# Optimization experiments

Measured on AMD Instinct MI355X. Metric: run time of the kernel, lower is better.

## Reference

```python
import jax, jax.numpy as jnp
import numpy as np

N_NODES = 50000
N_EDGES = 800000
N_GRAPHS = 64
EMB_DIM = 24
N_KERNELS = 2
M_DIM = 64
FOURIER = 4
POS_DIM = 3
EDGE_IN = 2 * FOURIER + 1 + 2 * EMB_DIM  # 57
MLP_DIM = 256
N_OUT = 4
FFNN_IN = EMB_DIM * (N_KERNELS + 1)  # 72


def _lin(key, fan_in, fan_out, stack=None):
    # xavier-uniform weight, zero bias (matches weights_init)
    lim = (6.0 / (fan_in + fan_out)) ** 0.5
    shp = ((stack,) if stack else ()) + (fan_in, fan_out)
    w = jax.random.uniform(key, shp, minval=-lim, maxval=lim, dtype=jnp.float32)
    b = jnp.zeros(((stack,) if stack else ()) + (fan_out,), jnp.float32)
    return w, b


def setup_inputs() -> dict:
    key = jax.random.key(0)
    ks = jax.random.split(key, 20)
    z = jax.random.randint(ks[0], (N_NODES,), 0, 22)
    pos = jax.random.normal(ks[1], (N_NODES, POS_DIM), jnp.float32)
    edge_index = jax.random.randint(ks[2], (2, N_EDGES), 0, N_NODES)
    batch_idx = jnp.sort(jax.random.randint(ks[3], (N_NODES,), 0, N_GRAPHS))
    lim_e = (6.0 / (22 + EMB_DIM)) ** 0.5
    emb_table = jax.random.uniform(ks[4], (22, EMB_DIM), minval=-lim_e, maxval=lim_e, dtype=jnp.float32)
    emb_w, emb_b = _lin(ks[5], EMB_DIM, EMB_DIM)
    # EGNN kernel params, stacked over N_KERNELS
    ew1, eb1 = _lin(ks[6], EDGE_IN, EDGE_IN * 2, N_KERNELS)
    ew2, eb2 = _lin(ks[7], EDGE_IN * 2, M_DIM, N_KERNELS)
    cw1, cb1 = _lin(ks[8], M_DIM, M_DIM * 4, N_KERNELS)
    cw2, cb2 = _lin(ks[9], M_DIM * 4, 1, N_KERNELS)
    nw1, nb1 = _lin(ks[10], EMB_DIM + M_DIM, EMB_DIM * 2, N_KERNELS)
    nw2, nb2 = _lin(ks[11], EMB_DIM * 2, EMB_DIM, N_KERNELS)
    # ffnn: Linear(72,256), Linear(256,256), Linear(256,256), Linear(256,4)
    f0w, f0b = _lin(ks[12], FFNN_IN, MLP_DIM)
    f1w, f1b = _lin(ks[13], MLP_DIM, MLP_DIM)
    f2w, f2b = _lin(ks[14], MLP_DIM, MLP_DIM)
    fow, fob = _lin(ks[15], MLP_DIM, N_OUT)
    return dict(z=z, pos=pos, edge_index=edge_index, batch_idx=batch_idx,
                emb_table=emb_table, emb_w=emb_w, emb_b=emb_b,
                ew1=ew1, eb1=eb1, ew2=ew2, eb2=eb2,
                cw1=cw1, cb1=cb1, cw2=cw2, cb2=cb2,
                nw1=nw1, nb1=nb1, nw2=nw2, nb2=nb2,
                f0w=f0w, f0b=f0b, f1w=f1w, f1b=f1b, f2w=f2w, f2b=f2b,
                fow=fow, fob=fob)


def _egnn_layer(feats, coors, src, dst, ew1, eb1, ew2, eb2, cw1, cb1, cw2, cb2, nw1, nb1, nw2, nb2):
    # EGNN_sparse (PyG flow source_to_target: i=dst=edge_index[1], j=src=edge_index[0])
    rel = coors[src] - coors[dst]                       # [E,3]
    d = jnp.sum(rel * rel, axis=-1, keepdims=True)      # [E,1] squared distance
    scales = 2.0 ** jnp.arange(FOURIER, dtype=feats.dtype)
    ds = d / scales                                     # [E,4]
    edge_feat = jnp.concatenate([jnp.sin(ds), jnp.cos(ds), d], axis=-1)  # [E,9]
    e_in = jnp.concatenate([feats[dst], feats[src], edge_feat], axis=-1)  # [E,57]
    m_ij = jax.nn.silu(jax.nn.silu(e_in @ ew1 + eb1) @ ew2 + eb2)         # [E,64]
    coor_w = jax.nn.silu(m_ij @ cw1 + cb1) @ cw2 + cb2                    # [E,1]
    coors_out = coors + jax.ops.segment_sum(coor_w * rel, dst, num_segments=N_NODES)
    m_i = jax.ops.segment_sum(m_ij, dst, num_segments=N_NODES)            # [N,64]
    h = jax.nn.silu(jnp.concatenate([feats, m_i], axis=-1) @ nw1 + nb1)
    feats_out = feats + (h @ nw2 + nb2)
    return feats_out, coors_out


def reference(z, pos, edge_index, batch_idx, emb_table, emb_w, emb_b,
              ew1, eb1, ew2, eb2, cw1, cb1, cw2, cb2, nw1, nb1, nw2, nb2,
              f0w, f0b, f1w, f1b, f2w, f2b, fow, fob):
    src, dst = edge_index[0], edge_index[1]
    feats = emb_table[z] @ emb_w + emb_b
    coors = pos
    flist = [feats]
    for k in range(N_KERNELS):
        feats, coors = _egnn_layer(feats, coors, src, dst,
                                   ew1[k], eb1[k], ew2[k], eb2[k],
                                   cw1[k], cb1[k], cw2[k], cb2[k],
                                   nw1[k], nb1[k], nw2[k], nb2[k])
        flist.append(feats)
    x = jax.nn.silu(jnp.concatenate(flist, axis=-1))     # [N,72]
    x = jax.nn.silu(x @ f0w + f0b)
    x = jax.nn.silu(x @ f1w + f1b)
    x = jax.nn.silu(x @ f2w + f2b)                       # [N,256]
    cnt = jax.ops.segment_sum(jnp.ones((x.shape[0],), x.dtype), batch_idx, num_segments=N_GRAPHS)
    pooled = jax.ops.segment_sum(x, batch_idx, num_segments=N_GRAPHS) / jnp.maximum(cnt, 1.0)[:, None]
    return jax.nn.sigmoid(pooled @ fow + fob)            # [B,4]
```

## Files before the change

### kernel.cpp

```cpp
#include <hip/hip_runtime.h>
#include <hip/hip_bf16.h>

#define N_NODES  50000
#define N_EDGES  800000
#define N_GRAPHS 64
#define EMB      24
#define MDIM     64
#define EDGE_IN  57
#define EH       114
#define CH       256
#define NIN      88
#define NH       48
#define MLP      256
#define ETILE    128
#define NTILE    64

typedef __bf16 bf16_t;
typedef __bf16 bf16x8 __attribute__((ext_vector_type(8)));
typedef __bf16 bf16x4 __attribute__((ext_vector_type(4)));
typedef float  f32x4  __attribute__((ext_vector_type(4)));

__device__ __forceinline__ float siluf(float x) {
    return x * __builtin_amdgcn_rcpf(1.0f + __expf(-x));
}

__global__ void embed_kernel(const int* __restrict__ z, const float* __restrict__ table,
                             const float* __restrict__ w, const float* __restrict__ b,
                             const int* __restrict__ batch, float* __restrict__ f0,
                             bf16_t* __restrict__ fb0, float* __restrict__ cnt)
{
    int n = blockIdx.x * blockDim.x + threadIdx.x;
    if (n >= N_NODES) return;
    float r[EMB];
    const float4* tr = reinterpret_cast<const float4*>(table + z[n] * EMB);
    #pragma unroll
    for (int q = 0; q < 6; q++) {
        float4 v = tr[q];
        r[q*4] = v.x; r[q*4+1] = v.y; r[q*4+2] = v.z; r[q*4+3] = v.w;
    }
    float o[EMB];
    #pragma unroll
    for (int j = 0; j < EMB; j++) o[j] = b[j];
    #pragma unroll
    for (int i = 0; i < EMB; i++) {
        #pragma unroll
        for (int j = 0; j < EMB; j++) o[j] = fmaf(r[i], w[i*EMB + j], o[j]);
    }
    float4* dst = reinterpret_cast<float4*>(f0 + (size_t)n * EMB);
    #pragma unroll
    for (int q = 0; q < 6; q++) dst[q] = make_float4(o[q*4], o[q*4+1], o[q*4+2], o[q*4+3]);
    bf16x8* bdst = reinterpret_cast<bf16x8*>(fb0 + (size_t)n * EMB);
    #pragma unroll
    for (int q = 0; q < 3; q++) {
        bf16x8 pk;
        #pragma unroll
        for (int j = 0; j < 8; j++) pk[j] = (bf16_t)o[q*8 + j];
        bdst[q] = pk;
    }
    atomicAdd(&cnt[batch[n]], 1.0f);
}

#define PK_W1   (128*64)
#define PK_W2   (64*128)
#define PK_CW   (256*64)
#define PK_F0   (256*128)
#define PK_FM   (256*256)
#define PK_TOT  (2*PK_W1 + 2*PK_W2 + PK_CW + PK_F0 + 2*PK_FM)
__global__ void pack_kernel(const float* __restrict__ ew1, const float* __restrict__ eb1,
                            const float* __restrict__ ew2, const float* __restrict__ eb2,
                            const float* __restrict__ cw1, const float* __restrict__ f0w,
                            const float* __restrict__ f1w, const float* __restrict__ f2w,
                            bf16_t* __restrict__ pw)
{
    int idx = blockIdx.x * blockDim.x + threadIdx.x;
    if (idx >= PK_TOT) return;
    float v = 0.0f;
    if (idx < 2 * PK_W1) {
        int l = idx / PK_W1, r = idx - l * PK_W1;
        int n = r >> 6, k = r & 63;
        if (n < EH && k < EDGE_IN)       v = ew1[(l * EDGE_IN + k) * EH + n];
        else if (n < EH && k == EDGE_IN) v = eb1[l * EH + n];
    } else if (idx < 2 * PK_W1 + 2 * PK_W2) {
        int r0 = idx - 2 * PK_W1;
        int l = r0 / PK_W2, r = r0 - l * PK_W2;
        int n = r >> 7, k = r & 127;
        if (k < EH)       v = ew2[(l * EH + k) * MDIM + n];
        else if (k == EH) v = eb2[l * MDIM + n];
    } else if (idx < 2 * PK_W1 + 2 * PK_W2 + PK_CW) {
        int r = idx - (2 * PK_W1 + 2 * PK_W2);
        int n = r >> 6, k = r & 63;
        v = cw1[k * CH + n];
    } else if (idx < 2 * PK_W1 + 2 * PK_W2 + PK_CW + PK_F0) {
        int r = idx - (2 * PK_W1 + 2 * PK_W2 + PK_CW);
        int n = r >> 7, k = r & 127;
        if (k < 72) v = f0w[k * MLP + n];
    } else {
        int r0 = idx - (2 * PK_W1 + 2 * PK_W2 + PK_CW + PK_F0);
        int l = r0 / PK_FM, r = r0 - l * PK_FM;
        int n = r >> 8, k = r & 255;
        v = (l == 0) ? f1w[k * MLP + n] : f2w[k * MLP + n];
    }
    pw[idx] = (bf16_t)v;
}

__global__ void hist_kernel(const int* __restrict__ dst, int* __restrict__ deg)
{
    int e = blockIdx.x * blockDim.x + threadIdx.x;
    if (e < N_EDGES) atomicAdd(&deg[dst[e]], 1);
}

__global__ __launch_bounds__(1024)
void scan_kernel(const int* __restrict__ deg, int* __restrict__ cursor)
{
    __shared__ int part[1024];
    int t = threadIdx.x;
    const int PER = 49;
    int base = t * PER;
    int s = 0;
    for (int i = 0; i < PER; i++) {
        int p = base + i;
        if (p < N_NODES) s += deg[p];
    }
    part[t] = s;
    __syncthreads();
    for (int off = 1; off < 1024; off <<= 1) {
        int add = (t >= off) ? part[t - off] : 0;
        __syncthreads();
        part[t] += add;
        __syncthreads();
    }
    int run = (t > 0) ? part[t - 1] : 0;
    for (int i = 0; i < PER; i++) {
        int p = base + i;
        if (p < N_NODES) { cursor[p] = run; run += deg[p]; }
    }
}

__global__ void scatter_kernel(const int* __restrict__ src, const int* __restrict__ dst,
                               int* __restrict__ cursor, int* __restrict__ srcs_s,
                               int* __restrict__ dsts_s)
{
    int e = blockIdx.x * blockDim.x + threadIdx.x;
    if (e >= N_EDGES) return;
    int d = dst[e];
    int pos = atomicAdd(&cursor[d], 1);
    srcs_s[pos] = src[e];
    dsts_s[pos] = d;
}

template<int COOR>
__global__ __launch_bounds__(256, 4)
void edge_mfma(const bf16_t* __restrict__ fb, const float* __restrict__ coors,
               const int* __restrict__ srcs_s, const int* __restrict__ dsts_s,
               const bf16_t* __restrict__ W1t, const bf16_t* __restrict__ W2t,
               const bf16_t* __restrict__ CW1t, const float* __restrict__ cb1,
               const float* __restrict__ cw2, const float* __restrict__ cb2,
               float* __restrict__ m_i, float* __restrict__ cdelta)
{
    __shared__ __align__(16) char R1raw[ETILE * 64 * 4];
    __shared__ float s_rel[COOR ? ETILE * 3 : 4];
    __shared__ int   s_dst[ETILE];
    bf16_t* R1 = (bf16_t*)R1raw;
    float*  Mf32 = (float*)R1raw;

    const int t = threadIdx.x;
    const int w = t >> 6;
    const int l = t & 63;
    const int row0 = w * 32;
    const int ebase = blockIdx.x * ETILE;
    const int l15 = l & 15, l4 = l >> 4;

    {
        int e_loc = t >> 1, half = t & 1;
        int e = ebase + e_loc;
        int s = srcs_s[e], d = dsts_s[e];
        if (half == 0) {
            s_dst[e_loc] = d;
            const bf16x8* fp = reinterpret_cast<const bf16x8*>(fb + (size_t)d * EMB);
            #pragma unroll
            for (int g = 0; g < 3; g++)
                *(bf16x8*)&R1[e_loc*64 + (g ^ (e_loc & 7))*8] = fp[g];
        } else {
            const bf16x8* fp = reinterpret_cast<const bf16x8*>(fb + (size_t)s * EMB);
            #pragma unroll
            for (int g = 0; g < 3; g++)
                *(bf16x8*)&R1[e_loc*64 + ((g + 3) ^ (e_loc & 7))*8] = fp[g];
            float rx = coors[s*3+0] - coors[d*3+0];
            float ry = coors[s*3+1] - coors[d*3+1];
            float rz = coors[s*3+2] - coors[d*3+2];
            float d2 = rx*rx + ry*ry + rz*rz;
            if (COOR) { s_rel[e_loc*3+0] = rx; s_rel[e_loc*3+1] = ry; s_rel[e_loc*3+2] = rz; }
            bf16x8 p6, p7;
            p6[0]=(bf16_t)__sinf(d2);        p6[1]=(bf16_t)__sinf(d2*0.5f);
            p6[2]=(bf16_t)__sinf(d2*0.25f);  p6[3]=(bf16_t)__sinf(d2*0.125f);
            p6[4]=(bf16_t)__cosf(d2);        p6[5]=(bf16_t)__cosf(d2*0.5f);
            p6[6]=(bf16_t)__cosf(d2*0.25f);  p6[7]=(bf16_t)__cosf(d2*0.125f);
            p7[0]=(bf16_t)d2; p7[1]=(bf16_t)1.0f;
            p7[2]=(bf16_t)0.f; p7[3]=(bf16_t)0.f; p7[4]=(bf16_t)0.f;
            p7[5]=(bf16_t)0.f; p7[6]=(bf16_t)0.f; p7[7]=(bf16_t)0.f;
            *(bf16x8*)&R1[e_loc*64 + (6 ^ (e_loc & 7))*8] = p6;
            *(bf16x8*)&R1[e_loc*64 + (7 ^ (e_loc & 7))*8] = p7;
        }
    }
    __syncthreads();

    f32x4 acc1[2][8];
    #pragma unroll
    for (int et = 0; et < 2; et++)
        #pragma unroll
        for (int ft = 0; ft < 8; ft++) acc1[et][ft] = (f32x4){0.f,0.f,0.f,0.f};
    #pragma unroll
    for (int ks = 0; ks < 2; ks++) {
        bf16x8 bfrag[2];
        #pragma unroll
        for (int et = 0; et < 2; et++) {
            int e = row0 + et*16 + l15;
            bfrag[et] = *(const bf16x8*)&R1[e*64 + ((ks*4 + l4) ^ (e & 7))*8];
        }
        #pragma unroll
        for (int ft = 0; ft < 8; ft++) {
            bf16x8 a = *(const bf16x8*)&W1t[(ft*16 + l15)*64 + (ks*4 + l4)*8];
            acc1[0][ft] = __builtin_amdgcn_mfma_f32_16x16x32_bf16(a, bfrag[0], acc1[0][ft], 0, 0, 0);
            acc1[1][ft] = __builtin_amdgcn_mfma_f32_16x16x32_bf16(a, bfrag[1], acc1[1][ft], 0, 0, 0);
        }
    }
    __syncthreads();
    #pragma unroll
    for (int et = 0; et < 2; et++)
        #pragma unroll
        for (int ft = 0; ft < 8; ft++) {
            int e = row0 + et*16 + l15;
            int f0 = ft*16 + l4*4;
            bf16x4 pk;
            #pragma unroll
            for (int r4 = 0; r4 < 4; r4++) {
                float hv = siluf(acc1[et][ft][r4]);
                if (f0 + r4 == EH) hv = 1.0f;
                pk[r4] = (bf16_t)hv;
            }
            *(bf16x4*)&R1[e*128 + ((f0 >> 3) ^ (e & 7))*8 + (f0 & 7)] = pk;
        }
    __syncthreads();

    f32x4 acc2[2][4];
    #pragma unroll
    for (int et = 0; et < 2; et++)
        #pragma unroll
        for (int ft = 0; ft < 4; ft++) acc2[et][ft] = (f32x4){0.f,0.f,0.f,0.f};
    #pragma unroll
    for (int ks = 0; ks < 4; ks++) {
        bf16x8 bfrag[2];
        #pragma unroll
        for (int et = 0; et < 2; et++) {
            int e = row0 + et*16 + l15;
            bfrag[et] = *(const bf16x8*)&R1[e*128 + ((ks*4 + l4) ^ (e & 7))*8];
        }
        #pragma unroll
        for (int ft = 0; ft < 4; ft++) {
            bf16x8 a = *(const bf16x8*)&W2t[(ft*16 + l15)*128 + (ks*4 + l4)*8];
            acc2[0][ft] = __builtin_amdgcn_mfma_f32_16x16x32_bf16(a, bfrag[0], acc2[0][ft], 0, 0, 0);
            acc2[1][ft] = __builtin_amdgcn_mfma_f32_16x16x32_bf16(a, bfrag[1], acc2[1][ft], 0, 0, 0);
        }
    }
    __syncthreads();
    #pragma unroll
    for (int et = 0; et < 2; et++)
        #pragma unroll
        for (int ft = 0; ft < 4; ft++) {
            int e = row0 + et*16 + l15;
            int f0 = ft*16 + l4*4;
            f32x4 v;
            #pragma unroll
            for (int r4 = 0; r4 < 4; r4++) v[r4] = siluf(acc2[et][ft][r4]);
            *(f32x4*)&Mf32[e*64 + (((f0 >> 2) ^ (e & 7)) << 2)] = v;
        }
    __syncthreads();

    {
        int col = t & 63;
        int gsw_base = col >> 2, cw = col & 3;
        int gb = w * 32;
        int cur = s_dst[gb];
        float run = 0.f;
        for (int i = 0; i < 32; i++) {
            int row = gb + i;
            int d = s_dst[row];
            float v = Mf32[row*64 + ((gsw_base ^ (row & 7)) << 2) + cw];
            if (d != cur) { atomicAdd(&m_i[(size_t)cur*64 + col], run); run = 0.f; cur = d; }
            run += v;
        }
        atomicAdd(&m_i[(size_t)cur*64 + col], run);
    }

    if (COOR) {
        float csum[2] = {0.f, 0.f};
        #pragma unroll
        for (int half = 0; half < 2; half++) {
            f32x4 acc3[2][8];
            #pragma unroll
            for (int et = 0; et < 2; et++)
                #pragma unroll
                for (int ft = 0; ft < 8; ft++) acc3[et][ft] = (f32x4){0.f,0.f,0.f,0.f};
            #pragma unroll
            for (int ks = 0; ks < 2; ks++) {
                bf16x8 bfrag[2];
                #pragma unroll
                for (int et = 0; et < 2; et++) {
                    int e = row0 + et*16 + l15;
                    int g0 = (ks*4 + l4) * 2;
                    f32x4 lo = *(const f32x4*)&Mf32[e*64 + ((g0 ^ (e & 7)) << 2)];
                    f32x4 hi = *(const f32x4*)&Mf32[e*64 + (((g0 + 1) ^ (e & 7)) << 2)];
                    bf16x8 bk;
                    #pragma unroll
                    for (int j = 0; j < 4; j++) { bk[j] = (bf16_t)lo[j]; bk[j+4] = (bf16_t)hi[j]; }
                    bfrag[et] = bk;
                }
                #pragma unroll
                for (int ft = 0; ft < 8; ft++) {
                    bf16x8 a = *(const bf16x8*)&CW1t[(half*128 + ft*16 + l15)*64 + (ks*4 + l4)*8];
                    acc3[0][ft] = __builtin_amdgcn_mfma_f32_16x16x32_bf16(a, bfrag[0], acc3[0][ft], 0, 0, 0);
                    acc3[1][ft] = __builtin_amdgcn_mfma_f32_16x16x32_bf16(a, bfrag[1], acc3[1][ft], 0, 0, 0);
                }
            }
            #pragma unroll
            for (int ft = 0; ft < 8; ft++) {
                int f0 = half*128 + ft*16 + l4*4;
                float4 c1 = *(const float4*)&cb1[f0];
                float4 w2 = *(const float4*)&cw2[f0];
                #pragma unroll
                for (int et = 0; et < 2; et++) {
                    csum[et] = fmaf(siluf(acc3[et][ft][0] + c1.x), w2.x, csum[et]);
                    csum[et] = fmaf(siluf(acc3[et][ft][1] + c1.y), w2.y, csum[et]);
                    csum[et] = fmaf(siluf(acc3[et][ft][2] + c1.z), w2.z, csum[et]);
                    csum[et] = fmaf(siluf(acc3[et][ft][3] + c1.w), w2.w, csum[et]);
                }
            }
        }
        #pragma unroll
        for (int et = 0; et < 2; et++) {
            csum[et] += __shfl_xor(csum[et], 16);
            csum[et] += __shfl_xor(csum[et], 32);
        }
        if (l < 16) {
            float cb2v = cb2[0];
            #pragma unroll
            for (int et = 0; et < 2; et++) {
                int row = row0 + et*16 + l;
                float cacc = csum[et] + cb2v;
                int d = s_dst[row];
                atomicAdd(&cdelta[d*3+0], cacc * s_rel[row*3+0]);
                atomicAdd(&cdelta[d*3+1], cacc * s_rel[row*3+1]);
                atomicAdd(&cdelta[d*3+2], cacc * s_rel[row*3+2]);
            }
        }
    }
}

template<int EMIT_BF16>
__global__ __launch_bounds__(256)
void node_kernel(const float* __restrict__ feats, const float* __restrict__ m_i,
                 const float* __restrict__ nw1, const float* __restrict__ nb1,
                 const float* __restrict__ nw2, const float* __restrict__ nb2,
                 float* __restrict__ fout, bf16_t* __restrict__ fbout)
{
    __shared__ float s_w1t[NH * NIN];
    __shared__ float s_b1[NH];
    __shared__ float s_w2[NH * EMB];
    __shared__ float s_b2[EMB];
    const int tid = threadIdx.x;
    for (int idx = tid; idx < NH * NIN; idx += 256) {
        int k = idx / NIN, i = idx - k * NIN;
        s_w1t[idx] = nw1[i * NH + k];
    }
    for (int idx = tid; idx < NH * EMB; idx += 256) s_w2[idx] = nw2[idx];
    if (tid < NH) s_b1[tid] = nb1[tid];
    if (tid < EMB) s_b2[tid] = nb2[tid];
    __syncthreads();

    int n = blockIdx.x * 256 + tid;
    if (n >= N_NODES) return;

    float in[NIN];
    const float4* fp = reinterpret_cast<const float4*>(feats + (size_t)n * EMB);
    #pragma unroll
    for (int q = 0; q < 6; q++) {
        float4 v = fp[q];
        in[q*4] = v.x; in[q*4+1] = v.y; in[q*4+2] = v.z; in[q*4+3] = v.w;
    }
    const float4* mp = reinterpret_cast<const float4*>(m_i + (size_t)n * MDIM);
    #pragma unroll
    for (int q = 0; q < 16; q++) {
        float4 v = mp[q];
        in[EMB+q*4] = v.x; in[EMB+q*4+1] = v.y; in[EMB+q*4+2] = v.z; in[EMB+q*4+3] = v.w;
    }
    float o[EMB];
    #pragma unroll
    for (int j = 0; j < EMB; j++) o[j] = in[j] + s_b2[j];
    for (int k = 0; k < NH; k++) {
        const float* w1 = &s_w1t[k * NIN];
        float a0 = 0.f, a1 = 0.f, a2 = 0.f, a3 = 0.f;
        #pragma unroll
        for (int i = 0; i < NIN; i += 4) {
            a0 = fmaf(in[i],   w1[i],   a0);
            a1 = fmaf(in[i+1], w1[i+1], a1);
            a2 = fmaf(in[i+2], w1[i+2], a2);
            a3 = fmaf(in[i+3], w1[i+3], a3);
        }
        float h = siluf(s_b1[k] + ((a0 + a1) + (a2 + a3)));
        const float* w2 = &s_w2[k * EMB];
        #pragma unroll
        for (int j = 0; j < EMB; j++) o[j] = fmaf(h, w2[j], o[j]);
    }
    float4* dst = reinterpret_cast<float4*>(fout + (size_t)n * EMB);
    #pragma unroll
    for (int q = 0; q < 6; q++) dst[q] = make_float4(o[q*4], o[q*4+1], o[q*4+2], o[q*4+3]);
    if (EMIT_BF16) {
        bf16x8* bdst = reinterpret_cast<bf16x8*>(fbout + (size_t)n * EMB);
        #pragma unroll
        for (int q = 0; q < 3; q++) {
            bf16x8 pk;
            #pragma unroll
            for (int j = 0; j < 8; j++) pk[j] = (bf16_t)o[q*8 + j];
            bdst[q] = pk;
        }
    }
}

__global__ void coor_kernel(const float* __restrict__ pos, const float* __restrict__ cdelta,
                            float* __restrict__ out)
{
    int i = blockIdx.x * blockDim.x + threadIdx.x;
    if (i < N_NODES * 3) out[i] = pos[i] + cdelta[i];
}

__global__ __launch_bounds__(256, 4)
void ffnn_fused(const float* __restrict__ f0, const float* __restrict__ f1,
                const float* __restrict__ f2,
                const bf16_t* __restrict__ W0p, const bf16_t* __restrict__ W1p,
                const bf16_t* __restrict__ W2p,
                const float* __restrict__ b0, const float* __restrict__ b1,
                const float* __restrict__ b2,
                const int* __restrict__ batch, float* __restrict__ pooled)
{
    __shared__ __align__(16) bf16_t sH[NTILE * 256];
    __shared__ int s_batch[NTILE];
    const int t = threadIdx.x;
    const int w = t >> 6, l = t & 63;
    const int row0 = w * 16;
    const int n0 = blockIdx.x * NTILE;

    {
        int row = t >> 2, part = t & 3;
        int n = n0 + row;
        bool valid = n < N_NODES;
        if (part == 3) s_batch[row] = valid ? batch[n] : -1;
        #pragma unroll
        for (int gi = 0; gi < 4; gi++) {
            int g = part * 4 + gi;
            bf16x8 pk;
            #pragma unroll
            for (int j = 0; j < 8; j++) pk[j] = (bf16_t)0.f;
            if (valid && g < 9) {
                const float* sp = (g < 3) ? f0 + (size_t)n*EMB + 8*g
                                : (g < 6) ? f1 + (size_t)n*EMB + 8*(g-3)
                                          : f2 + (size_t)n*EMB + 8*(g-6);
                float4 a = ((const float4*)sp)[0], b = ((const float4*)sp)[1];
                pk[0]=(bf16_t)siluf(a.x); pk[1]=(bf16_t)siluf(a.y);
                pk[2]=(bf16_t)siluf(a.z); pk[3]=(bf16_t)siluf(a.w);
                pk[4]=(bf16_t)siluf(b.x); pk[5]=(bf16_t)siluf(b.y);
                pk[6]=(bf16_t)siluf(b.z); pk[7]=(bf16_t)siluf(b.w);
            }
            *(bf16x8*)&sH[row*128 + (g ^ (row & 7))*8] = pk;
        }
    }
    __syncthreads();

    bf16x8 a0[4];
    {
        int r = row0 + (l & 15);
        #pragma unroll
        for (int ks = 0; ks < 4; ks++)
            a0[ks] = *(const bf16x8*)&sH[r*128 + ((ks*4 + (l >> 4)) ^ (r & 7))*8];
    }
    __syncthreads();

    f32x4 acc[16];
    #pragma unroll
    for (int nt = 0; nt < 16; nt++) {
        float bv = b0[nt*16 + (l & 15)];
        acc[nt] = (f32x4){bv, bv, bv, bv};
    }
    #pragma unroll
    for (int ks = 0; ks < 4; ks++)
        #pragma unroll
        for (int nt = 0; nt < 16; nt++) {
            int n = nt*16 + (l & 15);
            bf16x8 b = *(const bf16x8*)&W0p[n*128 + (ks*4 + (l >> 4))*8];
            acc[nt] = __builtin_amdgcn_mfma_f32_16x16x32_bf16(a0[ks], b, acc[nt], 0, 0, 0);
        }
    #pragma unroll
    for (int nt = 0; nt < 16; nt++)
        #pragma unroll
        for (int r4 = 0; r4 < 4; r4++) {
            int row = row0 + (l >> 4)*4 + r4;
            int col = nt*16 + (l & 15);
            sH[row*256 + ((col >> 3) ^ (row & 7))*8 + (col & 7)] = (bf16_t)siluf(acc[nt][r4]);
        }
    __syncthreads();

    #pragma unroll
    for (int layer = 0; layer < 2; layer++) {
        const bf16_t* Wp = layer ? W2p : W1p;
        const float*  bb = layer ? b2  : b1;
        #pragma unroll
        for (int nt = 0; nt < 16; nt++) {
            float bv = bb[nt*16 + (l & 15)];
            acc[nt] = (f32x4){bv, bv, bv, bv};
        }
        for (int ks = 0; ks < 8; ks++) {
            int r = row0 + (l & 15);
            bf16x8 a = *(const bf16x8*)&sH[r*256 + ((ks*4 + (l >> 4)) ^ (r & 7))*8];
            #pragma unroll
            for (int nt = 0; nt < 16; nt++) {
                int n = nt*16 + (l & 15);
                bf16x8 b = *(const bf16x8*)&Wp[n*256 + (ks*4 + (l >> 4))*8];
                acc[nt] = __builtin_amdgcn_mfma_f32_16x16x32_bf16(a, b, acc[nt], 0, 0, 0);
            }
        }
        __syncthreads();
        #pragma unroll
        for (int nt = 0; nt < 16; nt++)
            #pragma unroll
            for (int r4 = 0; r4 < 4; r4++) {
                int row = row0 + (l >> 4)*4 + r4;
                int col = nt*16 + (l & 15);
                sH[row*256 + ((col >> 3) ^ (row & 7))*8 + (col & 7)] = (bf16_t)siluf(acc[nt][r4]);
            }
        __syncthreads();
    }

    {
        int j = t;
        int g = j >> 3, jo = j & 7;
        int cur = -1;
        float run = 0.f;
        for (int i = 0; i < NTILE; i++) {
            int bb = s_batch[i];
            if (bb != cur) {
                if (cur >= 0) atomicAdd(&pooled[cur * MLP + j], run);
                run = 0.f; cur = bb;
            }
            if (bb >= 0) run += (float)sH[i*256 + (g ^ (i & 7))*8 + jo];
        }
        if (cur >= 0) atomicAdd(&pooled[cur * MLP + j], run);
    }
}

__global__ void final_kernel(const float* __restrict__ pooled, const float* __restrict__ cnt,
                             const float* __restrict__ fow, const float* __restrict__ fob,
                             float* __restrict__ out)
{
    int t = threadIdx.x;
    int bg = t >> 2, o = t & 3;
    float c = fmaxf(cnt[bg], 1.0f);
    float acc = 0.f;
    for (int i = 0; i < MLP; i++) acc = fmaf(pooled[bg * MLP + i], fow[i * 4 + o], acc);
    acc = acc / c + fob[o];
    out[t] = 1.0f / (1.0f + __expf(-acc));
}

extern "C" void kernel_launch(void* const* d_in, const int* in_sizes, int n_in,
                              void* d_out, int out_size, void* d_ws, size_t ws_size,
                              hipStream_t stream)
{
    const int*   z     = (const int*)  d_in[0];
    const float* pos   = (const float*)d_in[1];
    const int*   eidx  = (const int*)  d_in[2];
    const int*   batch = (const int*)  d_in[3];
    const float* embt  = (const float*)d_in[4];
    const float* embw  = (const float*)d_in[5];
    const float* embb  = (const float*)d_in[6];
    const float* ew1   = (const float*)d_in[7];
    const float* eb1   = (const float*)d_in[8];
    const float* ew2   = (const float*)d_in[9];
    const float* eb2   = (const float*)d_in[10];
    const float* cw1   = (const float*)d_in[11];
    const float* cb1   = (const float*)d_in[12];
    const float* cw2   = (const float*)d_in[13];
    const float* cb2   = (const float*)d_in[14];
    const float* nw1   = (const float*)d_in[15];
    const float* nb1   = (const float*)d_in[16];
    const float* nw2   = (const float*)d_in[17];
    const float* nb2   = (const float*)d_in[18];
    const float* f0w   = (const float*)d_in[19];
    const float* f0b   = (const float*)d_in[20];
    const float* f1w   = (const float*)d_in[21];
    const float* f1b   = (const float*)d_in[22];
    const float* f2w   = (const float*)d_in[23];
    const float* f2b   = (const float*)d_in[24];
    const float* fow   = (const float*)d_in[25];
    const float* fob   = (const float*)d_in[26];

    float* ws     = (float*)d_ws;
    float* f0     = ws;
    float* f1v    = f0 + (size_t)N_NODES * EMB;
    float* f2v    = f1v + (size_t)N_NODES * EMB;
    bf16_t* fb0   = (bf16_t*)(f2v + (size_t)N_NODES * EMB);
    bf16_t* fb1   = fb0 + (size_t)N_NODES * EMB;
    float* coorsA = (float*)(fb1 + (size_t)N_NODES * EMB);
    float* cdelta = coorsA + N_NODES * 3;
    float* m_i    = cdelta + N_NODES * 3;
    float* pooled = m_i + (size_t)N_NODES * MDIM;
    float* cnt    = pooled + N_GRAPHS * MLP;
    int*   deg    = (int*)(cnt + N_GRAPHS);
    int*   cursor = deg + N_NODES;
    int*   srcs_s = cursor + N_NODES;
    int*   dsts_s = srcs_s + N_EDGES;
    bf16_t* packw = (bf16_t*)(dsts_s + N_EDGES);
    bf16_t* W1t0  = packw;
    bf16_t* W1t1  = W1t0 + PK_W1;
    bf16_t* W2t0  = W1t1 + PK_W1;
    bf16_t* W2t1  = W2t0 + PK_W2;
    bf16_t* CW1t  = W2t1 + PK_W2;
    bf16_t* W0p   = CW1t + PK_CW;
    bf16_t* W1p   = W0p + PK_F0;
    bf16_t* W2p   = W1p + PK_FM;

    hipMemsetAsync(cdelta, 0, N_NODES * 3 * sizeof(float), stream);
    hipMemsetAsync(m_i, 0, (size_t)N_NODES * MDIM * sizeof(float), stream);
    hipMemsetAsync(pooled, 0, (N_GRAPHS * MLP + N_GRAPHS) * sizeof(float), stream);
    hipMemsetAsync(deg, 0, N_NODES * sizeof(int), stream);

    const int* e_src = eidx;
    const int* e_dst = eidx + N_EDGES;
    pack_kernel<<<(PK_TOT + 255) / 256, 256, 0, stream>>>(ew1, eb1, ew2, eb2, cw1,
                                                          f0w, f1w, f2w, packw);
    hist_kernel<<<(N_EDGES + 255) / 256, 256, 0, stream>>>(e_dst, deg);
    scan_kernel<<<1, 1024, 0, stream>>>(deg, cursor);
    scatter_kernel<<<(N_EDGES + 255) / 256, 256, 0, stream>>>(e_src, e_dst, cursor, srcs_s, dsts_s);

    embed_kernel<<<(N_NODES + 255) / 256, 256, 0, stream>>>(z, embt, embw, embb, batch, f0, fb0, cnt);

    const int EBLK = N_EDGES / ETILE;
    edge_mfma<1><<<EBLK, 256, 0, stream>>>(fb0, pos, srcs_s, dsts_s,
        W1t0, W2t0, CW1t, cb1, cw2, cb2, m_i, cdelta);
    node_kernel<1><<<(N_NODES + 255) / 256, 256, 0, stream>>>(f0, m_i, nw1, nb1, nw2, nb2, f1v, fb1);
    coor_kernel<<<(N_NODES * 3 + 255) / 256, 256, 0, stream>>>(pos, cdelta, coorsA);
    hipMemsetAsync(m_i, 0, (size_t)N_NODES * MDIM * sizeof(float), stream);
    edge_mfma<0><<<EBLK, 256, 0, stream>>>(fb1, coorsA, srcs_s, dsts_s,
        W1t1, W2t1, CW1t, cb1, cw2, cb2, m_i, nullptr);
    node_kernel<0><<<(N_NODES + 255) / 256, 256, 0, stream>>>(f1v, m_i,
        nw1 + NIN * NH, nb1 + NH, nw2 + NH * EMB, nb2 + EMB, f2v, nullptr);

    const int FBLK = (N_NODES + NTILE - 1) / NTILE;
    ffnn_fused<<<FBLK, 256, 0, stream>>>(f0, f1v, f2v, W0p, W1p, W2p,
                                         f0b, f1b, f2b, batch, pooled);

    final_kernel<<<1, 256, 0, stream>>>(pooled, cnt, fow, fob, (float*)d_out);
}
```

Measured before the change: 1.105 ms.

## Aggregate coordinate atomics per destination run and split FFNN N-tiles across 8 waves

The coordinate-update path in the first edge kernel now stores per-edge coefficients to shared memory. The first edge of each run of equal destinations (edges are sorted by destination) sums the whole run and issues one atomic per component, which cuts global atomic traffic. The fused FFNN kernel goes from 256 to 512 threads: each wave handles 8 of 16 output column tiles for a 16-row slice, halving accumulator registers, and pooling is split over two row halves. The tradeoffs are an extra block barrier and a serial run-scan in the edge kernel, plus more barrier cost and duplicated A-fragment loads in the FFNN.

```diff
diff --git a/kernel.cpp b/kernel.cpp
--- a/kernel.cpp
+++ b/kernel.cpp
@@ -159,6 +159,7 @@
 {
     __shared__ __align__(16) char R1raw[ETILE * 64 * 4];
     __shared__ float s_rel[COOR ? ETILE * 3 : 4];
+    __shared__ float s_cacc[COOR ? ETILE : 4];
     __shared__ int   s_dst[ETILE];
     bf16_t* R1 = (bf16_t*)R1raw;
     float*  Mf32 = (float*)R1raw;
@@ -343,14 +344,26 @@
         }
         if (l < 16) {
             float cb2v = cb2[0];
-            #pragma unroll
-            for (int et = 0; et < 2; et++) {
-                int row = row0 + et*16 + l;
-                float cacc = csum[et] + cb2v;
-                int d = s_dst[row];
-                atomicAdd(&cdelta[d*3+0], cacc * s_rel[row*3+0]);
-                atomicAdd(&cdelta[d*3+1], cacc * s_rel[row*3+1]);
-                atomicAdd(&cdelta[d*3+2], cacc * s_rel[row*3+2]);
+            s_cacc[row0 + l]      = csum[0] + cb2v;
+            s_cacc[row0 + 16 + l] = csum[1] + cb2v;
+        }
+        __syncthreads();
+        if (t < ETILE) {
+            int d = s_dst[t];
+            bool head = (t == 0) || (s_dst[t-1] != d);
+            if (head) {
+                float ax = 0.f, ay = 0.f, az = 0.f;
+                int i = t;
+                do {
+                    float c = s_cacc[i];
+                    ax = fmaf(c, s_rel[i*3+0], ax);
+                    ay = fmaf(c, s_rel[i*3+1], ay);
+                    az = fmaf(c, s_rel[i*3+2], az);
+                    ++i;
+                } while (i < ETILE && s_dst[i] == d);
+                atomicAdd(&cdelta[d*3+0], ax);
+                atomicAdd(&cdelta[d*3+1], ay);
+                atomicAdd(&cdelta[d*3+2], az);
             }
         }
     }
@@ -433,7 +446,7 @@
     if (i < N_NODES * 3) out[i] = pos[i] + cdelta[i];
 }
 
-__global__ __launch_bounds__(256, 4)
+__global__ __launch_bounds__(512, 4)
 void ffnn_fused(const float* __restrict__ f0, const float* __restrict__ f1,
                 const float* __restrict__ f2,
                 const bf16_t* __restrict__ W0p, const bf16_t* __restrict__ W1p,
@@ -446,17 +459,20 @@
     __shared__ int s_batch[NTILE];
     const int t = threadIdx.x;
     const int w = t >> 6, l = t & 63;
-    const int row0 = w * 16;
+    const int l15 = l & 15, q = l >> 4;
+    const int mt = w & 3;
+    const int nh = w >> 2;
+    const int mrow0 = mt * 16;
     const int n0 = blockIdx.x * NTILE;
 
     {
-        int row = t >> 2, part = t & 3;
+        int row = t >> 3, part = t & 7;
         int n = n0 + row;
         bool valid = n < N_NODES;
-        if (part == 3) s_batch[row] = valid ? batch[n] : -1;
-        #pragma unroll
-        for (int gi = 0; gi < 4; gi++) {
-            int g = part * 4 + gi;
+        if (part == 7) s_batch[row] = valid ? batch[n] : -1;
+        #pragma unroll
+        for (int gi = 0; gi < 2; gi++) {
+            int g = part * 2 + gi;
             bf16x8 pk;
             #pragma unroll
             for (int j = 0; j < 8; j++) pk[j] = (bf16_t)0.f;
@@ -477,33 +493,33 @@
 
     bf16x8 a0[4];
     {
-        int r = row0 + (l & 15);
+        int r = mrow0 + l15;
         #pragma unroll
         for (int ks = 0; ks < 4; ks++)
-            a0[ks] = *(const bf16x8*)&sH[r*128 + ((ks*4 + (l >> 4)) ^ (r & 7))*8];
-    }
-    __syncthreads();
-
-    f32x4 acc[16];
-    #pragma unroll
-    for (int nt = 0; nt < 16; nt++) {
-        float bv = b0[nt*16 + (l & 15)];
+            a0[ks] = *(const bf16x8*)&sH[r*128 + ((ks*4 + q) ^ (r & 7))*8];
+    }
+    __syncthreads();
+
+    f32x4 acc[8];
+    #pragma unroll
+    for (int nt = 0; nt < 8; nt++) {
+        float bv = b0[(nh*8 + nt)*16 + l15];
         acc[nt] = (f32x4){bv, bv, bv, bv};
     }
     #pragma unroll
     for (int ks = 0; ks < 4; ks++)
         #pragma unroll
-        for (int nt = 0; nt < 16; nt++) {
-            int n = nt*16 + (l & 15);
-            bf16x8 b = *(const bf16x8*)&W0p[n*128 + (ks*4 + (l >> 4))*8];
+        for (int nt = 0; nt < 8; nt++) {
+            int n = (nh*8 + nt)*16 + l15;
+            bf16x8 b = *(const bf16x8*)&W0p[n*128 + (ks*4 + q)*8];
             acc[nt] = __builtin_amdgcn_mfma_f32_16x16x32_bf16(a0[ks], b, acc[nt], 0, 0, 0);
         }
     #pragma unroll
-    for (int nt = 0; nt < 16; nt++)
+    for (int nt = 0; nt < 8; nt++)
         #pragma unroll
         for (int r4 = 0; r4 < 4; r4++) {
-            int row = row0 + (l >> 4)*4 + r4;
-            int col = nt*16 + (l & 15);
+            int row = mrow0 + q*4 + r4;
+            int col = (nh*8 + nt)*16 + l15;
             sH[row*256 + ((col >> 3) ^ (row & 7))*8 + (col & 7)] = (bf16_t)siluf(acc[nt][r4]);
         }
     __syncthreads();
@@ -513,38 +529,39 @@
         const bf16_t* Wp = layer ? W2p : W1p;
         const float*  bb = layer ? b2  : b1;
         #pragma unroll
-        for (int nt = 0; nt < 16; nt++) {
-            float bv = bb[nt*16 + (l & 15)];
+        for (int nt = 0; nt < 8; nt++) {
+            float bv = bb[(nh*8 + nt)*16 + l15];
             acc[nt] = (f32x4){bv, bv, bv, bv};
         }
         for (int ks = 0; ks < 8; ks++) {
-            int r = row0 + (l & 15);
-            bf16x8 a = *(const bf16x8*)&sH[r*256 + ((ks*4 + (l >> 4)) ^ (r & 7))*8];
-            #pragma unroll
-            for (int nt = 0; nt < 16; nt++) {
-                int n = nt*16 + (l & 15);
-                bf16x8 b = *(const bf16x8*)&Wp[n*256 + (ks*4 + (l >> 4))*8];
+            int r = mrow0 + l15;
+            bf16x8 a = *(const bf16x8*)&sH[r*256 + ((ks*4 + q) ^ (r & 7))*8];
+            #pragma unroll
+            for (int nt = 0; nt < 8; nt++) {
+                int n = (nh*8 + nt)*16 + l15;
+                bf16x8 b = *(const bf16x8*)&Wp[n*256 + (ks*4 + q)*8];
                 acc[nt] = __builtin_amdgcn_mfma_f32_16x16x32_bf16(a, b, acc[nt], 0, 0, 0);
             }
         }
         __syncthreads();
         #pragma unroll
-        for (int nt = 0; nt < 16; nt++)
+        for (int nt = 0; nt < 8; nt++)
             #pragma unroll
             for (int r4 = 0; r4 < 4; r4++) {
-                int row = row0 + (l >> 4)*4 + r4;
-                int col = nt*16 + (l & 15);
+                int row = mrow0 + q*4 + r4;
+                int col = (nh*8 + nt)*16 + l15;
                 sH[row*256 + ((col >> 3) ^ (row & 7))*8 + (col & 7)] = (bf16_t)siluf(acc[nt][r4]);
             }
         __syncthreads();
     }
 
     {
-        int j = t;
+        int j = t & 255;
+        int rh = t >> 8;
         int g = j >> 3, jo = j & 7;
         int cur = -1;
         float run = 0.f;
-        for (int i = 0; i < NTILE; i++) {
+        for (int i = rh*32; i < rh*32 + 32; i++) {
             int bb = s_batch[i];
             if (bb != cur) {
                 if (cur >= 0) atomicAdd(&pooled[cur * MLP + j], run);
@@ -653,7 +670,7 @@
         nw1 + NIN * NH, nb1 + NH, nw2 + NH * EMB, nb2 + EMB, f2v, nullptr);
 
     const int FBLK = (N_NODES + NTILE - 1) / NTILE;
-    ffnn_fused<<<FBLK, 256, 0, stream>>>(f0, f1v, f2v, W0p, W1p, W2p,
+    ffnn_fused<<<FBLK, 512, 0, stream>>>(f0, f1v, f2v, W0p, W1p, W2p,
                                          f0b, f1b, f2b, batch, pooled);
 
     final_kernel<<<1, 256, 0, stream>>>(pooled, cnt, fow, fob, (float*)d_out);
```

Measured after the change: 995.4 us. -9.9%, faster.
